# Kernel optimization log

Hardware: AMD Instinct MI355X
Metric: run time of the kernel (lower is better)

## Reference

```python
import jax, jax.numpy as jnp
import numpy as np

N_NODES = 50000
N_EDGES = 800000
D_IN = 128
D_OUT = 128


def setup_inputs() -> dict:
    key = jax.random.key(0)
    k1, k2, k3, k4, k5 = jax.random.split(key, 5)
    x = jax.random.normal(k1, (N_NODES, D_IN), dtype=jnp.float32)
    w = jax.random.normal(k2, (D_IN, D_OUT), dtype=jnp.float32) * (1.0 / np.sqrt(D_IN))
    adj_rows = jnp.sort(jax.random.randint(k3, (N_EDGES,), 0, N_NODES, dtype=jnp.int32))
    adj_cols = jax.random.randint(k4, (N_EDGES,), 0, N_NODES, dtype=jnp.int32)
    adj_vals = jax.random.uniform(k5, (N_EDGES,), dtype=jnp.float32)
    return {"x": x, "w": w, "adj_rows": adj_rows, "adj_cols": adj_cols, "adj_vals": adj_vals}


def reference(x, w, adj_rows, adj_cols, adj_vals):
    # dense feature transform: [N, D_in] @ [D_in, D_out] -> [N, D_out]
    h = jnp.matmul(x, w)
    # sparse adjacency propagation (SpMM in COO form):
    # out[r] = sum over edges (r, c, v) of v * h[c]
    msg = adj_vals[:, None] * h[adj_cols]          # [E, D_out] gather
    out = jax.ops.segment_sum(msg, adj_rows, num_segments=x.shape[0])
    # activation (relu), fused into output pass
    return jax.nn.relu(out)
```

## Files before the change

kernel.cpp:

```cpp
#include <hip/hip_runtime.h>
#include <hip/hip_bf16.h>

#define D 128
#define GEMM_ROWS 32

typedef __bf16 bf16x8 __attribute__((ext_vector_type(8)));
typedef float  f32x4  __attribute__((ext_vector_type(4)));
typedef unsigned int u32x4 __attribute__((ext_vector_type(4)));

__device__ inline bf16x8 cvt_a8(const float* __restrict__ p) {
    float4 v0 = ((const float4*)p)[0], v1 = ((const float4*)p)[1];
    bf16x8 a;
    a[0] = (__bf16)v0.x; a[1] = (__bf16)v0.y; a[2] = (__bf16)v0.z; a[3] = (__bf16)v0.w;
    a[4] = (__bf16)v1.x; a[5] = (__bf16)v1.y; a[6] = (__bf16)v1.z; a[7] = (__bf16)v1.w;
    return a;
}

__global__ __launch_bounds__(256) void fused_gemm_rp(
        const float* __restrict__ x, const float* __restrict__ w,
        const int* __restrict__ rows,
        unsigned short* __restrict__ h, int* __restrict__ rp,
        int n_nodes, int n_edges, int gemm_blocks) {
    const int b = blockIdx.x;

    if (b >= gemm_blocks) {
        int e = (b - gemm_blocks) * 256 + threadIdx.x;
        if (e >= n_edges) return;
        int r    = rows[e];
        int prev = (e == 0) ? -1 : rows[e - 1];
        for (int rr = prev + 1; rr <= r; ++rr) rp[rr] = e;
        if (e == n_edges - 1)
            for (int rr = r + 1; rr <= n_nodes; ++rr) rp[rr] = n_edges;
        return;
    }

    const int wave = threadIdx.x >> 6;
    const int lane = threadIdx.x & 63;
    const int m16  = lane & 15;
    const int q    = lane >> 4;

    const int row0 = b * 64;
    const int col0 = wave * 32;

    bf16x8 bfr[2][4];
#pragma unroll
    for (int t = 0; t < 2; ++t)
#pragma unroll
        for (int s = 0; s < 4; ++s) {
            const float* wp = w + (size_t)(32 * s + q * 8) * D + col0 + 16 * t + m16;
#pragma unroll
            for (int j = 0; j < 8; ++j)
                bfr[t][s][j] = (__bf16)wp[(size_t)j * D];
        }

#pragma unroll 1
    for (int sl = 0; sl < 4; ++sl) {
        const int r = row0 + sl * 16 + m16;
        const float* xp = x + (size_t)r * D + q * 8;

        bf16x8 a[4];
        if (r < n_nodes) {
#pragma unroll
            for (int s = 0; s < 4; ++s) a[s] = cvt_a8(xp + 32 * s);
        } else {
#pragma unroll
            for (int s = 0; s < 4; ++s)
#pragma unroll
                for (int j = 0; j < 8; ++j) a[s][j] = (__bf16)0.f;
        }

        f32x4 acc0 = (f32x4)0.f, acc1 = (f32x4)0.f;
#pragma unroll
        for (int s = 0; s < 4; ++s) {
            acc0 = __builtin_amdgcn_mfma_f32_16x16x32_bf16(a[s], bfr[0][s], acc0, 0, 0, 0);
            acc1 = __builtin_amdgcn_mfma_f32_16x16x32_bf16(a[s], bfr[1][s], acc1, 0, 0, 0);
        }

#pragma unroll
        for (int i = 0; i < 4; ++i) {
            int row = row0 + sl * 16 + q * 4 + i;
            h[(size_t)row * D + col0 + m16]      = __builtin_bit_cast(unsigned short, (__bf16)acc0[i]);
            h[(size_t)row * D + col0 + 16 + m16] = __builtin_bit_cast(unsigned short, (__bf16)acc1[i]);
        }
    }
}

#define FMA8(hv, vv)                                                              \
    _Pragma("unroll")                                                             \
    for (int j = 0; j < 4; ++j) {                                                 \
        unsigned int u = (hv)[j];                                                 \
        acc[2 * j]     = fmaf((vv), __builtin_bit_cast(float, u << 16),           \
                              acc[2 * j]);                                        \
        acc[2 * j + 1] = fmaf((vv), __builtin_bit_cast(float, u & 0xFFFF0000u),   \
                              acc[2 * j + 1]);                                    \
    }

__global__ __launch_bounds__(256) void spmm_bf16_b4(
        const unsigned short* __restrict__ h,
        const int* __restrict__ row_ptr,
        const int* __restrict__ cols,
        const float* __restrict__ vals,
        float* __restrict__ out, int n) {
    const int wave = threadIdx.x >> 6;
    const int lane = threadIdx.x & 63;
    const int r = blockIdx.x * 4 + wave;
    if (r >= n) return;

    const int start = row_ptr[r];
    const int end   = row_ptr[r + 1];
    const int chain = lane >> 4;
    const int l4    = lane & 15;

    const u32x4* h4 = (const u32x4*)h;
    float acc[8];
#pragma unroll
    for (int j = 0; j < 8; ++j) acc[j] = 0.f;

    int e = start + chain;
    int c0 = 0, c1 = 0, c2 = 0, c3 = 0;
    float v0 = 0.f, v1 = 0.f, v2 = 0.f, v3 = 0.f;
    if (e < end)      { c0 = cols[e];      v0 = vals[e]; }
    if (e + 4 < end)  { c1 = cols[e + 4];  v1 = vals[e + 4]; }
    if (e + 8 < end)  { c2 = cols[e + 8];  v2 = vals[e + 8]; }
    if (e + 12 < end) { c3 = cols[e + 12]; v3 = vals[e + 12]; }

    while (e < end) {
        int en = e + 16;
        int cn0 = 0, cn1 = 0, cn2 = 0, cn3 = 0;
        float vn0 = 0.f, vn1 = 0.f, vn2 = 0.f, vn3 = 0.f;
        if (en < end)      { cn0 = cols[en];      vn0 = vals[en]; }
        if (en + 4 < end)  { cn1 = cols[en + 4];  vn1 = vals[en + 4]; }
        if (en + 8 < end)  { cn2 = cols[en + 8];  vn2 = vals[en + 8]; }
        if (en + 12 < end) { cn3 = cols[en + 12]; vn3 = vals[en + 12]; }

        u32x4 hv0 = h4[(size_t)c0 * (D / 8) + l4];
        u32x4 hv1 = h4[(size_t)c1 * (D / 8) + l4];
        u32x4 hv2 = h4[(size_t)c2 * (D / 8) + l4];
        u32x4 hv3 = h4[(size_t)c3 * (D / 8) + l4];

        FMA8(hv0, v0)
        FMA8(hv1, v1)
        FMA8(hv2, v2)
        FMA8(hv3, v3)

        c0 = cn0; v0 = vn0; c1 = cn1; v1 = vn1;
        c2 = cn2; v2 = vn2; c3 = cn3; v3 = vn3;
        e = en;
    }

#pragma unroll
    for (int j = 0; j < 8; ++j) {
        acc[j] += __shfl_xor(acc[j], 16);
        acc[j] += __shfl_xor(acc[j], 32);
    }

    if (chain == 0) {
        float4 o0, o1;
        o0.x = fmaxf(acc[0], 0.f); o0.y = fmaxf(acc[1], 0.f);
        o0.z = fmaxf(acc[2], 0.f); o0.w = fmaxf(acc[3], 0.f);
        o1.x = fmaxf(acc[4], 0.f); o1.y = fmaxf(acc[5], 0.f);
        o1.z = fmaxf(acc[6], 0.f); o1.w = fmaxf(acc[7], 0.f);
        float4* op = (float4*)(out + (size_t)r * D + l4 * 8);
        op[0] = o0; op[1] = o1;
    }
}

__global__ __launch_bounds__(256) void gemm128(const float* __restrict__ x,
                                               const float* __restrict__ w,
                                               float* __restrict__ h, int n) {
    __shared__ float4 ws4[D * D / 4];
    __shared__ float  xs[GEMM_ROWS][D];
    const int tid  = threadIdx.x;
    const int row0 = blockIdx.x * GEMM_ROWS;
    const float4* w4 = (const float4*)w;
    for (int i = tid; i < D * D / 4; i += 256) ws4[i] = w4[i];
    float4* xs4 = (float4*)&xs[0][0];
    const float4* x4 = (const float4*)x;
    for (int i = tid; i < GEMM_ROWS * D / 4; i += 256) {
        int row = row0 + (i >> 5);
        float4 v = make_float4(0.f, 0.f, 0.f, 0.f);
        if (row < n) v = x4[(size_t)row0 * (D / 4) + i];
        xs4[i] = v;
    }
    __syncthreads();
    const int tx = tid & 31, ty = tid >> 5;
    float4 acc[4];
#pragma unroll
    for (int i = 0; i < 4; ++i) acc[i] = make_float4(0.f, 0.f, 0.f, 0.f);
#pragma unroll 8
    for (int k = 0; k < D; ++k) {
        float4 wv = ws4[k * (D / 4) + tx];
#pragma unroll
        for (int i = 0; i < 4; ++i) {
            float xv = xs[ty * 4 + i][k];
            acc[i].x = fmaf(xv, wv.x, acc[i].x);
            acc[i].y = fmaf(xv, wv.y, acc[i].y);
            acc[i].z = fmaf(xv, wv.z, acc[i].z);
            acc[i].w = fmaf(xv, wv.w, acc[i].w);
        }
    }
#pragma unroll
    for (int i = 0; i < 4; ++i) {
        int row = row0 + ty * 4 + i;
        if (row < n) ((float4*)(h + (size_t)row * D))[tx] = acc[i];
    }
}

__global__ __launch_bounds__(128) void spmm_row(const float* __restrict__ h,
                                                const int* __restrict__ rows,
                                                const int* __restrict__ cols,
                                                const float* __restrict__ vals,
                                                float* __restrict__ out, int n_edges) {
    const int r = blockIdx.x, d = threadIdx.x;
    int lo = 0, hi = n_edges;
    while (lo < hi) { int m = (lo + hi) >> 1; if (rows[m] < r) lo = m + 1; else hi = m; }
    const int start = lo;
    hi = n_edges;
    while (lo < hi) { int m = (lo + hi) >> 1; if (rows[m] <= r) lo = m + 1; else hi = m; }
    const int end = lo;
    float acc = 0.f;
    for (int e = start; e < end; ++e)
        acc = fmaf(vals[e], h[(size_t)cols[e] * D + d], acc);
    out[(size_t)r * D + d] = fmaxf(acc, 0.f);
}

__global__ __launch_bounds__(128) void fused_fallback(
        const float* __restrict__ x, const float* __restrict__ w,
        const int* __restrict__ rows, const int* __restrict__ cols,
        const float* __restrict__ vals, float* __restrict__ out, int n_edges) {
    const int r = blockIdx.x, d = threadIdx.x;
    int lo = 0, hi = n_edges;
    while (lo < hi) { int m = (lo + hi) >> 1; if (rows[m] < r) lo = m + 1; else hi = m; }
    const int start = lo;
    hi = n_edges;
    while (lo < hi) { int m = (lo + hi) >> 1; if (rows[m] <= r) lo = m + 1; else hi = m; }
    const int end = lo;
    float acc = 0.f;
    for (int e = start; e < end; ++e) {
        int c = cols[e]; float v = vals[e];
        float hcd = 0.f;
        for (int k = 0; k < D; ++k)
            hcd = fmaf(x[(size_t)c * D + k], w[(size_t)k * D + d], hcd);
        acc = fmaf(v, hcd, acc);
    }
    out[(size_t)r * D + d] = fmaxf(acc, 0.f);
}

extern "C" void kernel_launch(void* const* d_in, const int* in_sizes, int n_in,
                              void* d_out, int out_size, void* d_ws, size_t ws_size,
                              hipStream_t stream) {
    const float* x    = (const float*)d_in[0];
    const float* w    = (const float*)d_in[1];
    const int*   rows = (const int*)d_in[2];
    const int*   cols = (const int*)d_in[3];
    const float* vals = (const float*)d_in[4];
    float* out = (float*)d_out;

    const int n_nodes = in_sizes[0] / D;
    const int n_edges = in_sizes[2];
    const int n_pad   = (n_nodes + 63) & ~63;

    const size_t h_bytes  = (size_t)n_pad * D * sizeof(unsigned short);
    const size_t rp_off   = h_bytes;
    const size_t need     = rp_off + (size_t)(n_nodes + 1) * sizeof(int);
    const size_t hf_bytes = (size_t)n_nodes * D * sizeof(float);

    if (ws_size >= need) {
        unsigned short* h  = (unsigned short*)d_ws;
        int*            rp = (int*)((char*)d_ws + rp_off);

        const int gemm_blocks = n_pad / 64;
        const int rp_blocks   = (n_edges + 255) / 256;
        fused_gemm_rp<<<gemm_blocks + rp_blocks, 256, 0, stream>>>(
            x, w, rows, h, rp, n_nodes, n_edges, gemm_blocks);

        spmm_bf16_b4<<<(n_nodes + 3) / 4, 256, 0, stream>>>(h, rp, cols, vals, out, n_nodes);
    } else if (ws_size >= hf_bytes) {
        float* hf = (float*)d_ws;
        gemm128<<<(n_nodes + GEMM_ROWS - 1) / GEMM_ROWS, 256, 0, stream>>>(x, w, hf, n_nodes);
        spmm_row<<<n_nodes, 128, 0, stream>>>(hf, rows, cols, vals, out, n_edges);
    } else {
        fused_fallback<<<n_nodes, 128, 0, stream>>>(x, w, rows, cols, vals, out, n_edges);
    }
}
```

Measured before the change: 126.7 us.

## Fuse GEMM, row-pointer build and SpMM into one persistent kernel with grid barrier

Replaces the two-kernel pipeline with a single persistent kernel of 1024 blocks. Each block grid-strides over GEMM tiles and edge row-pointer construction, then waits at a software grid barrier (atomic counter reset by a memset) before each wave handles a contiguous chunk of rows in the SpMM. The aim is to remove a kernel launch boundary and its tail. In exchange it adds a memset launch and a spin barrier that assumes all 1024 blocks are co-resident, and the static row chunking may balance load worse than one wave per row.

```diff
diff --git a/kernel.cpp b/kernel.cpp
--- a/kernel.cpp
+++ b/kernel.cpp
@@ -2,6 +2,7 @@
 #include <hip/hip_bf16.h>
 
 #define D 128
+#define NBLK 1024
 #define GEMM_ROWS 32
 
 typedef __bf16 bf16x8 __attribute__((ext_vector_type(8)));
@@ -16,74 +17,97 @@
     return a;
 }
 
-__global__ __launch_bounds__(256) void fused_gemm_rp(
+__global__ __launch_bounds__(256, 4) void gcn_fused(
         const float* __restrict__ x, const float* __restrict__ w,
-        const int* __restrict__ rows,
+        const int* __restrict__ rows, const int* __restrict__ cols,
+        const float* __restrict__ vals,
         unsigned short* __restrict__ h, int* __restrict__ rp,
-        int n_nodes, int n_edges, int gemm_blocks) {
-    const int b = blockIdx.x;
-
-    if (b >= gemm_blocks) {
-        int e = (b - gemm_blocks) * 256 + threadIdx.x;
-        if (e >= n_edges) return;
+        int* __restrict__ cnt, float* __restrict__ out,
+        int n_nodes, int n_edges) {
+    const int b    = blockIdx.x;
+    const int tid  = threadIdx.x;
+    const int wave = tid >> 6;
+    const int lane = tid & 63;
+    const int m16  = lane & 15;
+    const int q    = lane >> 4;
+
+    const int n_pad = (n_nodes + 63) & ~63;
+    const int tiles = n_pad >> 6;
+    const int col0  = wave * 32;
+
+    if (b < tiles) {
+        bf16x8 bfr[2][4];
+#pragma unroll
+        for (int t = 0; t < 2; ++t)
+#pragma unroll
+            for (int s = 0; s < 4; ++s) {
+                const float* wp = w + (size_t)(32 * s + q * 8) * D + col0 + 16 * t + m16;
+#pragma unroll
+                for (int j = 0; j < 8; ++j)
+                    bfr[t][s][j] = (__bf16)wp[(size_t)j * D];
+            }
+
+        for (int tile = b; tile < tiles; tile += NBLK) {
+            const int row0 = tile * 64;
+#pragma unroll 1
+            for (int sl = 0; sl < 4; ++sl) {
+                const int r = row0 + sl * 16 + m16;
+                const float* xp = x + (size_t)r * D + q * 8;
+
+                bf16x8 a[4];
+                if (r < n_nodes) {
+#pragma unroll
+                    for (int s = 0; s < 4; ++s) a[s] = cvt_a8(xp + 32 * s);
+                } else {
+#pragma unroll
+                    for (int s = 0; s < 4; ++s)
+#pragma unroll
+                        for (int j = 0; j < 8; ++j) a[s][j] = (__bf16)0.f;
+                }
+
+                f32x4 acc0 = (f32x4)0.f, acc1 = (f32x4)0.f;
+#pragma unroll
+                for (int s = 0; s < 4; ++s) {
+                    acc0 = __builtin_amdgcn_mfma_f32_16x16x32_bf16(a[s], bfr[0][s], acc0, 0, 0, 0);
+                    acc1 = __builtin_amdgcn_mfma_f32_16x16x32_bf16(a[s], bfr[1][s], acc1, 0, 0, 0);
+                }
+
+#pragma unroll
+                for (int i = 0; i < 4; ++i) {
+                    int row = row0 + sl * 16 + q * 4 + i;
+                    h[(size_t)row * D + col0 + m16]      = __builtin_bit_cast(unsigned short, (__bf16)acc0[i]);
+                    h[(size_t)row * D + col0 + 16 + m16] = __builtin_bit_cast(unsigned short, (__bf16)acc1[i]);
+                }
+            }
+        }
+    }
+
+    for (int e = b * 256 + tid; e < n_edges; e += NBLK * 256) {
         int r    = rows[e];
         int prev = (e == 0) ? -1 : rows[e - 1];
         for (int rr = prev + 1; rr <= r; ++rr) rp[rr] = e;
         if (e == n_edges - 1)
             for (int rr = r + 1; rr <= n_nodes; ++rr) rp[rr] = n_edges;
-        return;
-    }
-
-    const int wave = threadIdx.x >> 6;
-    const int lane = threadIdx.x & 63;
-    const int m16  = lane & 15;
-    const int q    = lane >> 4;
-
-    const int row0 = b * 64;
-    const int col0 = wave * 32;
-
-    bf16x8 bfr[2][4];
-#pragma unroll
-    for (int t = 0; t < 2; ++t)
-#pragma unroll
-        for (int s = 0; s < 4; ++s) {
-            const float* wp = w + (size_t)(32 * s + q * 8) * D + col0 + 16 * t + m16;
-#pragma unroll
-            for (int j = 0; j < 8; ++j)
-                bfr[t][s][j] = (__bf16)wp[(size_t)j * D];
-        }
-
-#pragma unroll 1
-    for (int sl = 0; sl < 4; ++sl) {
-        const int r = row0 + sl * 16 + m16;
-        const float* xp = x + (size_t)r * D + q * 8;
-
-        bf16x8 a[4];
-        if (r < n_nodes) {
-#pragma unroll
-            for (int s = 0; s < 4; ++s) a[s] = cvt_a8(xp + 32 * s);
-        } else {
-#pragma unroll
-            for (int s = 0; s < 4; ++s)
-#pragma unroll
-                for (int j = 0; j < 8; ++j) a[s][j] = (__bf16)0.f;
-        }
-
-        f32x4 acc0 = (f32x4)0.f, acc1 = (f32x4)0.f;
-#pragma unroll
-        for (int s = 0; s < 4; ++s) {
-            acc0 = __builtin_amdgcn_mfma_f32_16x16x32_bf16(a[s], bfr[0][s], acc0, 0, 0, 0);
-            acc1 = __builtin_amdgcn_mfma_f32_16x16x32_bf16(a[s], bfr[1][s], acc1, 0, 0, 0);
-        }
-
-#pragma unroll
-        for (int i = 0; i < 4; ++i) {
-            int row = row0 + sl * 16 + q * 4 + i;
-            h[(size_t)row * D + col0 + m16]      = __builtin_bit_cast(unsigned short, (__bf16)acc0[i]);
-            h[(size_t)row * D + col0 + 16 + m16] = __builtin_bit_cast(unsigned short, (__bf16)acc1[i]);
-        }
-    }
-}
+    }
+
+    __threadfence();
+    __syncthreads();
+    if (tid == 0) {
+        __hip_atomic_fetch_add(cnt, 1, __ATOMIC_ACQ_REL, __HIP_MEMORY_SCOPE_AGENT);
+        while (__hip_atomic_load(cnt, __ATOMIC_ACQUIRE, __HIP_MEMORY_SCOPE_AGENT) < (int)gridDim.x)
+            __builtin_amdgcn_s_sleep(2);
+    }
+    __syncthreads();
+    __threadfence();
+
+    const int wid   = b * 4 + wave;
+    const int nw    = NBLK * 4;
+    const int chunk = (n_nodes + nw - 1) / nw;
+    const int rbeg  = wid * chunk;
+    const int rend  = (rbeg + chunk < n_nodes) ? rbeg + chunk : n_nodes;
+    const int chain = lane >> 4;
+    const int l4    = lane & 15;
+    const u32x4* h4 = (const u32x4*)h;
 
 #define FMA8(hv, vv)                                                              \
     _Pragma("unroll")                                                             \
@@ -95,74 +119,63 @@
                               acc[2 * j + 1]);                                    \
     }
 
-__global__ __launch_bounds__(256) void spmm_bf16_b4(
-        const unsigned short* __restrict__ h,
-        const int* __restrict__ row_ptr,
-        const int* __restrict__ cols,
-        const float* __restrict__ vals,
-        float* __restrict__ out, int n) {
-    const int wave = threadIdx.x >> 6;
-    const int lane = threadIdx.x & 63;
-    const int r = blockIdx.x * 4 + wave;
-    if (r >= n) return;
-
-    const int start = row_ptr[r];
-    const int end   = row_ptr[r + 1];
-    const int chain = lane >> 4;
-    const int l4    = lane & 15;
-
-    const u32x4* h4 = (const u32x4*)h;
-    float acc[8];
-#pragma unroll
-    for (int j = 0; j < 8; ++j) acc[j] = 0.f;
-
-    int e = start + chain;
-    int c0 = 0, c1 = 0, c2 = 0, c3 = 0;
-    float v0 = 0.f, v1 = 0.f, v2 = 0.f, v3 = 0.f;
-    if (e < end)      { c0 = cols[e];      v0 = vals[e]; }
-    if (e + 4 < end)  { c1 = cols[e + 4];  v1 = vals[e + 4]; }
-    if (e + 8 < end)  { c2 = cols[e + 8];  v2 = vals[e + 8]; }
-    if (e + 12 < end) { c3 = cols[e + 12]; v3 = vals[e + 12]; }
-
-    while (e < end) {
-        int en = e + 16;
-        int cn0 = 0, cn1 = 0, cn2 = 0, cn3 = 0;
-        float vn0 = 0.f, vn1 = 0.f, vn2 = 0.f, vn3 = 0.f;
-        if (en < end)      { cn0 = cols[en];      vn0 = vals[en]; }
-        if (en + 4 < end)  { cn1 = cols[en + 4];  vn1 = vals[en + 4]; }
-        if (en + 8 < end)  { cn2 = cols[en + 8];  vn2 = vals[en + 8]; }
-        if (en + 12 < end) { cn3 = cols[en + 12]; vn3 = vals[en + 12]; }
-
-        u32x4 hv0 = h4[(size_t)c0 * (D / 8) + l4];
-        u32x4 hv1 = h4[(size_t)c1 * (D / 8) + l4];
-        u32x4 hv2 = h4[(size_t)c2 * (D / 8) + l4];
-        u32x4 hv3 = h4[(size_t)c3 * (D / 8) + l4];
-
-        FMA8(hv0, v0)
-        FMA8(hv1, v1)
-        FMA8(hv2, v2)
-        FMA8(hv3, v3)
-
-        c0 = cn0; v0 = vn0; c1 = cn1; v1 = vn1;
-        c2 = cn2; v2 = vn2; c3 = cn3; v3 = vn3;
-        e = en;
-    }
-
-#pragma unroll
-    for (int j = 0; j < 8; ++j) {
-        acc[j] += __shfl_xor(acc[j], 16);
-        acc[j] += __shfl_xor(acc[j], 32);
-    }
-
-    if (chain == 0) {
-        float4 o0, o1;
-        o0.x = fmaxf(acc[0], 0.f); o0.y = fmaxf(acc[1], 0.f);
-        o0.z = fmaxf(acc[2], 0.f); o0.w = fmaxf(acc[3], 0.f);
-        o1.x = fmaxf(acc[4], 0.f); o1.y = fmaxf(acc[5], 0.f);
-        o1.z = fmaxf(acc[6], 0.f); o1.w = fmaxf(acc[7], 0.f);
-        float4* op = (float4*)(out + (size_t)r * D + l4 * 8);
-        op[0] = o0; op[1] = o1;
-    }
+    for (int r = rbeg; r < rend; ++r) {
+        const int start = rp[r];
+        const int end   = rp[r + 1];
+
+        float acc[8];
+#pragma unroll
+        for (int j = 0; j < 8; ++j) acc[j] = 0.f;
+
+        int e = start + chain;
+        int c0 = 0, c1 = 0, c2 = 0, c3 = 0;
+        float v0 = 0.f, v1 = 0.f, v2 = 0.f, v3 = 0.f;
+        if (e < end)      { c0 = cols[e];      v0 = vals[e]; }
+        if (e + 4 < end)  { c1 = cols[e + 4];  v1 = vals[e + 4]; }
+        if (e + 8 < end)  { c2 = cols[e + 8];  v2 = vals[e + 8]; }
+        if (e + 12 < end) { c3 = cols[e + 12]; v3 = vals[e + 12]; }
+
+        while (e < end) {
+            int en = e + 16;
+            int cn0 = 0, cn1 = 0, cn2 = 0, cn3 = 0;
+            float vn0 = 0.f, vn1 = 0.f, vn2 = 0.f, vn3 = 0.f;
+            if (en < end)      { cn0 = cols[en];      vn0 = vals[en]; }
+            if (en + 4 < end)  { cn1 = cols[en + 4];  vn1 = vals[en + 4]; }
+            if (en + 8 < end)  { cn2 = cols[en + 8];  vn2 = vals[en + 8]; }
+            if (en + 12 < end) { cn3 = cols[en + 12]; vn3 = vals[en + 12]; }
+
+            u32x4 hv0 = h4[(size_t)c0 * (D / 8) + l4];
+            u32x4 hv1 = h4[(size_t)c1 * (D / 8) + l4];
+            u32x4 hv2 = h4[(size_t)c2 * (D / 8) + l4];
+            u32x4 hv3 = h4[(size_t)c3 * (D / 8) + l4];
+
+            FMA8(hv0, v0)
+            FMA8(hv1, v1)
+            FMA8(hv2, v2)
+            FMA8(hv3, v3)
+
+            c0 = cn0; v0 = vn0; c1 = cn1; v1 = vn1;
+            c2 = cn2; v2 = vn2; c3 = cn3; v3 = vn3;
+            e = en;
+        }
+
+#pragma unroll
+        for (int j = 0; j < 8; ++j) {
+            acc[j] += __shfl_xor(acc[j], 16);
+            acc[j] += __shfl_xor(acc[j], 32);
+        }
+
+        if (chain == 0) {
+            float4 o0, o1;
+            o0.x = fmaxf(acc[0], 0.f); o0.y = fmaxf(acc[1], 0.f);
+            o0.z = fmaxf(acc[2], 0.f); o0.w = fmaxf(acc[3], 0.f);
+            o1.x = fmaxf(acc[4], 0.f); o1.y = fmaxf(acc[5], 0.f);
+            o1.z = fmaxf(acc[6], 0.f); o1.w = fmaxf(acc[7], 0.f);
+            float4* op = (float4*)(out + (size_t)r * D + l4 * 8);
+            op[0] = o0; op[1] = o1;
+        }
+    }
+#undef FMA8
 }
 
 __global__ __launch_bounds__(256) void gemm128(const float* __restrict__ x,
@@ -262,19 +275,19 @@
 
     const size_t h_bytes  = (size_t)n_pad * D * sizeof(unsigned short);
     const size_t rp_off   = h_bytes;
-    const size_t need     = rp_off + (size_t)(n_nodes + 1) * sizeof(int);
+    const size_t cnt_off  = rp_off + (size_t)(n_nodes + 1) * sizeof(int);
+    const size_t need     = cnt_off + sizeof(int);
     const size_t hf_bytes = (size_t)n_nodes * D * sizeof(float);
 
     if (ws_size >= need) {
         unsigned short* h  = (unsigned short*)d_ws;
         int*            rp = (int*)((char*)d_ws + rp_off);
-
-        const int gemm_blocks = n_pad / 64;
-        const int rp_blocks   = (n_edges + 255) / 256;
-        fused_gemm_rp<<<gemm_blocks + rp_blocks, 256, 0, stream>>>(
-            x, w, rows, h, rp, n_nodes, n_edges, gemm_blocks);
-
-        spmm_bf16_b4<<<(n_nodes + 3) / 4, 256, 0, stream>>>(h, rp, cols, vals, out, n_nodes);
+        int*            cnt = (int*)((char*)d_ws + cnt_off);
+
+        hipMemsetAsync(cnt, 0, sizeof(int), stream);
+
+        gcn_fused<<<NBLK, 256, 0, stream>>>(x, w, rows, cols, vals,
+                                            h, rp, cnt, out, n_nodes, n_edges);
     } else if (ws_size >= hf_bytes) {
         float* hf = (float*)d_ws;
         gemm128<<<(n_nodes + GEMM_ROWS - 1) / GEMM_ROWS, 256, 0, stream>>>(x, w, hf, n_nodes);
```

New measurement: 448.0 us. +253.6%, slower.
